# Performance work log

Measured on AMD Instinct MI355X. Metric: run time of the kernel, lower is better.

The kernel has to match this reference:

```python
import jax, jax.numpy as jnp
import numpy as np

MARGIN = 0.7
ITERS = 1000  # as hard-coded in ot_loss's log_optimal_transport call


def setup_inputs() -> dict:
    key = jax.random.key(0)
    k1, k2 = jax.random.split(key)
    # features: N x C x W x H  (query at index 0, 8 targets)
    x = jax.random.normal(k1, (9, 256, 32, 32), dtype=jnp.float32)
    # attention: N x W x H, strictly positive since it is logged directly
    att = jax.random.uniform(k2, (9, 32, 32), dtype=jnp.float32, minval=0.1, maxval=1.0)
    return {"x": x, "att": att, "label": 1}


def _ot_distance(x, att):
    N, C, W, H = x.shape
    m = W * H              # number of query locations
    n = (N - 1) * W * H    # number of target locations
    Q = x[0].reshape(C, m).T                                          # (m, C)
    T = x[1:].reshape(N - 1, C, m).transpose(0, 2, 1).reshape(n, C)   # (n, C)
    mu = att[0].reshape(m)      # query marginal
    nu = att[1:].reshape(n)     # target marginal
    # pairwise squared euclidean distances (m, n)
    M = (jnp.sum(Q * Q, axis=1)[:, None]
         + jnp.sum(T * T, axis=1)[None, :]
         - 2.0 * (Q @ T.T))
    log_mu = jnp.log(mu)
    log_nu = jnp.log(nu)

    def step(carry, _):
        u, v = carry
        u = log_mu - jax.nn.logsumexp(M + v[None, :], axis=1)
        v = log_nu - jax.nn.logsumexp(M + u[:, None], axis=0)
        return (u, v), None

    init = (jnp.zeros((m,), M.dtype), jnp.zeros((n,), M.dtype))
    (u, v), _ = jax.lax.scan(jax.checkpoint(step), init, None, length=ITERS)
    P = jnp.exp(M + u[:, None] + v[None, :])   # transport plan (m, n)
    # OT barycentric distance per query location, summed
    diff = mu[:, None] * Q - P @ T             # (m, C)
    return jnp.sqrt(jnp.sum(diff * diff, axis=1)).sum()


def reference(x, att, label):
    d = _ot_distance(x, att)
    if label:  # label is a concrete python int: positive pair
        return d
    return jnp.clip(MARGIN - d, 0.0, None)
```

## Files before the change

kernel.cpp:

```cpp
#include <hip/hip_runtime.h>
#include <math.h>

#define MR 1024
#define NC 8192
#define NCH 256
#define OT_ITERS 1000
#define IMG_STRIDE 262144

__device__ inline float wredMax(float v){
#pragma unroll
  for (int m = 32; m >= 1; m >>= 1) v = fmaxf(v, __shfl_xor(v, m, 64));
  return v;
}
__device__ inline float wredMin(float v){
#pragma unroll
  for (int m = 32; m >= 1; m >>= 1) v = fminf(v, __shfl_xor(v, m, 64));
  return v;
}
__device__ inline float wredSum(float v){
#pragma unroll
  for (int m = 32; m >= 1; m >>= 1) v += __shfl_xor(v, m, 64);
  return v;
}

__device__ inline unsigned fkey(float f){
  unsigned b = __float_as_uint(f);
  return (b & 0x80000000u) ? ~b : (b | 0x80000000u);
}
__device__ inline float funkey(unsigned k){
  return (k & 0x80000000u) ? __uint_as_float(k & 0x7fffffffu) : __uint_as_float(~k);
}

__global__ __launch_bounds__(256) void kPrep(const float* __restrict__ x,
                                             const float* __restrict__ att,
                                             float* __restrict__ qq, float* __restrict__ tt,
                                             float* __restrict__ logmu, float* __restrict__ lognu,
                                             float* __restrict__ u, float* __restrict__ v,
                                             float* __restrict__ acc, unsigned* __restrict__ prmI){
  int idx = blockIdx.x * 256 + threadIdx.x;
  if (idx < 9216){
    int img = idx >> 10, pos = idx & 1023;
    const float* p = x + img * IMG_STRIDE + pos;
    float s = 0.f;
#pragma unroll 8
    for (int c = 0; c < NCH; ++c){ float a = p[c * 1024]; s += a * a; }
    float lg = logf(att[idx]);
    if (img == 0){ qq[idx] = s;        logmu[idx] = lg; }
    else         { tt[idx - 1024] = s; lognu[idx - 1024] = lg; }
  }
  if (idx < MR) u[idx] = 0.f;
  if (idx < NC) v[idx] = 0.f;
  if (idx == 0){ *acc = 0.f; prmI[0] = 0xFFFFFFFFu; prmI[1] = 0u; }
}

__global__ __launch_bounds__(256) void kGemmM(const float* __restrict__ x,
                                              const float* __restrict__ qq,
                                              const float* __restrict__ tt,
                                              float* __restrict__ M,
                                              unsigned* __restrict__ prmI){
  __shared__ float As[16][68];
  __shared__ float Bs[16][68];
  __shared__ float smn[4], smx[4];
  int jb = blockIdx.x;
  int ib = blockIdx.y;
  int i0 = ib * 64;
  int j0 = jb * 64;
  int k  = j0 >> 10, p0 = j0 & 1023;
  const float* A = x + i0;
  const float* B = x + (1 + k) * IMG_STRIDE + p0;
  int tid = threadIdx.x;
  int lr = tid >> 4, lc = (tid & 15) * 4;
  int ty = tid >> 4, tx = tid & 15;
  float accv[4][4] = {};
  for (int kt = 0; kt < 16; ++kt){
    int c = kt * 16 + lr;
    float4 av = *(const float4*)(A + c * 1024 + lc);
    float4 bv = *(const float4*)(B + c * 1024 + lc);
    *(float4*)(&As[lr][lc]) = av;
    *(float4*)(&Bs[lr][lc]) = bv;
    __syncthreads();
#pragma unroll
    for (int kk = 0; kk < 16; ++kk){
      float4 a = *(const float4*)(&As[kk][ty * 4]);
      float4 b = *(const float4*)(&Bs[kk][tx * 4]);
      float ar[4] = {a.x, a.y, a.z, a.w};
      float br[4] = {b.x, b.y, b.z, b.w};
#pragma unroll
      for (int r = 0; r < 4; ++r)
#pragma unroll
        for (int cc = 0; cc < 4; ++cc) accv[r][cc] += ar[r] * br[cc];
    }
    __syncthreads();
  }
  float tmn = INFINITY, tmx = -INFINITY;
#pragma unroll
  for (int r = 0; r < 4; ++r){
    int i = i0 + ty * 4 + r;
    float qi = qq[i];
    float o[4];
#pragma unroll
    for (int cc = 0; cc < 4; ++cc){
      o[cc] = qi + tt[j0 + tx * 4 + cc] - 2.f * accv[r][cc];
      tmn = fminf(tmn, o[cc]); tmx = fmaxf(tmx, o[cc]);
    }
    float4 ov = { o[0], o[1], o[2], o[3] };
    *(float4*)(M + (long)i * NC + j0 + tx * 4) = ov;
  }
  int lane = tid & 63, w = tid >> 6;
  tmn = wredMin(tmn); tmx = wredMax(tmx);
  if (lane == 0){ smn[w] = tmn; smx[w] = tmx; }
  __syncthreads();
  if (tid == 0){
    float bmn = fminf(fminf(smn[0], smn[1]), fminf(smn[2], smn[3]));
    float bmx = fmaxf(fmaxf(smx[0], smx[1]), fmaxf(smx[2], smx[3]));
    atomicMin(&prmI[0], fkey(bmn));
    atomicMax(&prmI[1], fkey(bmx));
  }
}

__global__ __launch_bounds__(256) void kQuantTrans(const float* __restrict__ M,
                                                   unsigned short* __restrict__ Mq,
                                                   unsigned short* __restrict__ Mtq,
                                                   float* __restrict__ prm){
  __shared__ float tile[64][65];
  const unsigned* prmI = (const unsigned*)prm;
  float mn = funkey(prmI[0]);
  float mx = funkey(prmI[1]);
  float rng = mx - mn;
  float inv = (rng > 0.f) ? 65535.0f / rng : 0.f;
  float sc  = (rng > 0.f) ? rng / 65535.0f : 0.f;
  int i0 = blockIdx.y * 64;
  int j0 = blockIdx.x * 64;
  int t = threadIdx.x;
  int tc = t & 63, tr = t >> 6;
#pragma unroll
  for (int rr = 0; rr < 64; rr += 4)
    tile[rr + tr][tc] = M[(long)(i0 + rr + tr) * NC + j0 + tc];
  __syncthreads();
#pragma unroll
  for (int rr = 0; rr < 64; rr += 4){
    float a = tile[rr + tr][tc];
    int qa = (int)lrintf((a - mn) * inv);
    qa = qa < 0 ? 0 : (qa > 65535 ? 65535 : qa);
    Mq[(long)(i0 + rr + tr) * NC + j0 + tc] = (unsigned short)qa;
    float b = tile[tc][rr + tr];
    int qb = (int)lrintf((b - mn) * inv);
    qb = qb < 0 ? 0 : (qb > 65535 ? 65535 : qb);
    Mtq[(long)(j0 + rr + tr) * MR + i0 + tc] = (unsigned short)qb;
  }
  if (blockIdx.x == 0 && blockIdx.y == 0 && t == 0){ prm[2] = mn; prm[3] = sc; }
}

__global__ __launch_bounds__(256) void kUPassQ(const unsigned short* __restrict__ Mq,
                                               const float* __restrict__ v,
                                               const float* __restrict__ logmu,
                                               float* __restrict__ u,
                                               const float* __restrict__ prm){
  int b = blockIdx.x, tid = threadIdx.x;
  float mn = prm[2], s = prm[3];
  int r0 = 2 * b;
  const unsigned short* R0 = Mq + (long)r0 * NC;
  const unsigned short* R1 = R0 + NC;
  float t0[32], t1[32];
  float mx0 = -INFINITY, mx1 = -INFINITY;
#pragma unroll
  for (int kb = 0; kb < 4; ++kb){
    int cidx = kb * 2048 + tid * 8;
    uint4 qa = *(const uint4*)(R0 + cidx);
    uint4 qb = *(const uint4*)(R1 + cidx);
    float4 v0 = *(const float4*)(v + cidx);
    float4 v1 = *(const float4*)(v + cidx + 4);
    float a0 = fmaf(s, (float)(qa.x & 0xFFFFu), v0.x);
    float a1 = fmaf(s, (float)(qa.x >> 16),     v0.y);
    float a2 = fmaf(s, (float)(qa.y & 0xFFFFu), v0.z);
    float a3 = fmaf(s, (float)(qa.y >> 16),     v0.w);
    float a4 = fmaf(s, (float)(qa.z & 0xFFFFu), v1.x);
    float a5 = fmaf(s, (float)(qa.z >> 16),     v1.y);
    float a6 = fmaf(s, (float)(qa.w & 0xFFFFu), v1.z);
    float a7 = fmaf(s, (float)(qa.w >> 16),     v1.w);
    float c0 = fmaf(s, (float)(qb.x & 0xFFFFu), v0.x);
    float c1 = fmaf(s, (float)(qb.x >> 16),     v0.y);
    float c2 = fmaf(s, (float)(qb.y & 0xFFFFu), v0.z);
    float c3 = fmaf(s, (float)(qb.y >> 16),     v0.w);
    float c4 = fmaf(s, (float)(qb.z & 0xFFFFu), v1.x);
    float c5 = fmaf(s, (float)(qb.z >> 16),     v1.y);
    float c6 = fmaf(s, (float)(qb.w & 0xFFFFu), v1.z);
    float c7 = fmaf(s, (float)(qb.w >> 16),     v1.w);
    t0[kb*8+0]=a0; t0[kb*8+1]=a1; t0[kb*8+2]=a2; t0[kb*8+3]=a3;
    t0[kb*8+4]=a4; t0[kb*8+5]=a5; t0[kb*8+6]=a6; t0[kb*8+7]=a7;
    t1[kb*8+0]=c0; t1[kb*8+1]=c1; t1[kb*8+2]=c2; t1[kb*8+3]=c3;
    t1[kb*8+4]=c4; t1[kb*8+5]=c5; t1[kb*8+6]=c6; t1[kb*8+7]=c7;
    mx0 = fmaxf(mx0, fmaxf(fmaxf(fmaxf(a0,a1),fmaxf(a2,a3)), fmaxf(fmaxf(a4,a5),fmaxf(a6,a7))));
    mx1 = fmaxf(mx1, fmaxf(fmaxf(fmaxf(c0,c1),fmaxf(c2,c3)), fmaxf(fmaxf(c4,c5),fmaxf(c6,c7))));
  }
  __shared__ float redA0[4], redA1[4], redB0[4], redB1[4];
  int lane = tid & 63, w = tid >> 6;
  float wm0 = wredMax(mx0), wm1 = wredMax(mx1);
  if (lane == 0){ redA0[w] = wm0; redA1[w] = wm1; }
  __syncthreads();
  float bm0 = fmaxf(fmaxf(redA0[0], redA0[1]), fmaxf(redA0[2], redA0[3]));
  float bm1 = fmaxf(fmaxf(redA1[0], redA1[1]), fmaxf(redA1[2], redA1[3]));
  float s0 = 0.f, s1 = 0.f;
#pragma unroll
  for (int q = 0; q < 32; ++q){ s0 += __expf(t0[q] - bm0); s1 += __expf(t1[q] - bm1); }
  s0 = wredSum(s0); s1 = wredSum(s1);
  if (lane == 0){ redB0[w] = s0; redB1[w] = s1; }
  __syncthreads();
  if (tid == 0){
    u[r0]     = logmu[r0]     - mn - (bm0 + __logf(redB0[0] + redB0[1] + redB0[2] + redB0[3]));
    u[r0 + 1] = logmu[r0 + 1] - mn - (bm1 + __logf(redB1[0] + redB1[1] + redB1[2] + redB1[3]));
  }
}

__global__ __launch_bounds__(256) void kVPassQ(const unsigned short* __restrict__ Mtq,
                                               const float* __restrict__ u,
                                               const float* __restrict__ lognu,
                                               float* __restrict__ v,
                                               const float* __restrict__ prm){
  __shared__ float ulds[1024];
  int tid = threadIdx.x;
  float mn = prm[2], s = prm[3];
  *(float4*)(&ulds[tid * 4]) = *(const float4*)(u + tid * 4);
  __syncthreads();
  int w = tid >> 6, lane = tid & 63;
#pragma unroll
  for (int cc = 0; cc < 4; ++cc){
    int j = blockIdx.x * 16 + w * 4 + cc;
    const unsigned short* R = Mtq + (long)j * MR;
    uint4 qa = *(const uint4*)(R + lane * 8);
    uint4 qb = *(const uint4*)(R + 512 + lane * 8);
    float4 ua0 = *(const float4*)(&ulds[lane * 8]);
    float4 ua1 = *(const float4*)(&ulds[lane * 8 + 4]);
    float4 ub0 = *(const float4*)(&ulds[512 + lane * 8]);
    float4 ub1 = *(const float4*)(&ulds[512 + lane * 8 + 4]);
    float tv[16];
    tv[0]  = fmaf(s, (float)(qa.x & 0xFFFFu), ua0.x);
    tv[1]  = fmaf(s, (float)(qa.x >> 16),     ua0.y);
    tv[2]  = fmaf(s, (float)(qa.y & 0xFFFFu), ua0.z);
    tv[3]  = fmaf(s, (float)(qa.y >> 16),     ua0.w);
    tv[4]  = fmaf(s, (float)(qa.z & 0xFFFFu), ua1.x);
    tv[5]  = fmaf(s, (float)(qa.z >> 16),     ua1.y);
    tv[6]  = fmaf(s, (float)(qa.w & 0xFFFFu), ua1.z);
    tv[7]  = fmaf(s, (float)(qa.w >> 16),     ua1.w);
    tv[8]  = fmaf(s, (float)(qb.x & 0xFFFFu), ub0.x);
    tv[9]  = fmaf(s, (float)(qb.x >> 16),     ub0.y);
    tv[10] = fmaf(s, (float)(qb.y & 0xFFFFu), ub0.z);
    tv[11] = fmaf(s, (float)(qb.y >> 16),     ub0.w);
    tv[12] = fmaf(s, (float)(qb.z & 0xFFFFu), ub1.x);
    tv[13] = fmaf(s, (float)(qb.z >> 16),     ub1.y);
    tv[14] = fmaf(s, (float)(qb.w & 0xFFFFu), ub1.z);
    tv[15] = fmaf(s, (float)(qb.w >> 16),     ub1.w);
    float mx = -INFINITY;
#pragma unroll
    for (int q = 0; q < 16; ++q) mx = fmaxf(mx, tv[q]);
    mx = wredMax(mx);
    float sm = 0.f;
#pragma unroll
    for (int q = 0; q < 16; ++q) sm += __expf(tv[q] - mx);
    sm = wredSum(sm);
    if (lane == 0) v[j] = lognu[j] - mn - (mx + __logf(sm));
  }
}

__global__ __launch_bounds__(256) void kFinal(const float* __restrict__ x,
                                              const float* __restrict__ att,
                                              const float* __restrict__ M,
                                              const float* __restrict__ u,
                                              const float* __restrict__ v,
                                              float* __restrict__ acc){
  __shared__ float pch[4][256];
  __shared__ float redS[4];
  int tid = threadIdx.x;
  int r0 = blockIdx.x * 4;
  float u4[4];
#pragma unroll
  for (int rr = 0; rr < 4; ++rr) u4[rr] = u[r0 + rr];
  float o[4] = {0.f, 0.f, 0.f, 0.f};
  for (int jc = 0; jc < NC; jc += 256){
    float vv = v[jc + tid];
#pragma unroll
    for (int rr = 0; rr < 4; ++rr)
      pch[rr][tid] = __expf(M[(long)(r0 + rr) * NC + jc + tid] + u4[rr] + vv);
    __syncthreads();
    int k = jc >> 10;
    const float* Tp = x + (1 + k) * IMG_STRIDE + tid * 1024 + (jc & 1023);
    for (int jj = 0; jj < 256; jj += 4){
      float4 tv = *(const float4*)(Tp + jj);
      float tq[4] = {tv.x, tv.y, tv.z, tv.w};
#pragma unroll
      for (int q = 0; q < 4; ++q){
        o[0] += pch[0][jj + q] * tq[q];
        o[1] += pch[1][jj + q] * tq[q];
        o[2] += pch[2][jj + q] * tq[q];
        o[3] += pch[3][jj + q] * tq[q];
      }
    }
    __syncthreads();
  }
  int lane = tid & 63, wid = tid >> 6;
  float dtot = 0.f;
#pragma unroll
  for (int rr = 0; rr < 4; ++rr){
    float mu = att[r0 + rr];
    float qv = x[tid * 1024 + (r0 + rr)];
    float diff = mu * qv - o[rr];
    float wsum = wredSum(diff * diff);
    if (lane == 0) redS[wid] = wsum;
    __syncthreads();
    if (tid == 0) dtot += sqrtf(redS[0] + redS[1] + redS[2] + redS[3]);
    __syncthreads();
  }
  if (tid == 0) atomicAdd(acc, dtot);
}

__global__ void kOut(const float* __restrict__ acc, const int* __restrict__ label,
                     float* __restrict__ out){
  if (threadIdx.x == 0 && blockIdx.x == 0){
    float d = *acc;
    out[0] = (*label) ? d : fmaxf(0.7f - d, 0.f);
  }
}

extern "C" void kernel_launch(void* const* d_in, const int* in_sizes, int n_in,
                              void* d_out, int out_size, void* d_ws, size_t ws_size,
                              hipStream_t stream){
  const float* x   = (const float*)d_in[0];
  const float* att = (const float*)d_in[1];
  const int* label = (const int*)d_in[2];
  float* W = (float*)d_ws;
  float* out = (float*)d_out;

  float* M = W;
  unsigned short* Mq  = (unsigned short*)(W + 8388608);
  unsigned short* Mtq = (unsigned short*)(W + 8388608 + 4194304);
  float* S     = W + 16777216;
  float* qq    = S;
  float* tt    = qq + 1024;
  float* logmu = tt + 8192;
  float* lognu = logmu + 1024;
  float* u     = lognu + 8192;
  float* v     = u + 1024;
  float* acc   = v + 8192;
  float* prm   = acc + 1;
  unsigned* prmI = (unsigned*)prm;

  hipLaunchKernelGGL(kPrep, dim3(37), dim3(256), 0, stream, x, att, qq, tt, logmu, lognu, u, v, acc, prmI);
  hipLaunchKernelGGL(kGemmM, dim3(128, 16), dim3(256), 0, stream, x, qq, tt, M, prmI);
  hipLaunchKernelGGL(kQuantTrans, dim3(128, 16), dim3(256), 0, stream, M, Mq, Mtq, prm);
  for (int it = 0; it < OT_ITERS; ++it){
    hipLaunchKernelGGL(kUPassQ, dim3(512), dim3(256), 0, stream, Mq, v, logmu, u, prm);
    hipLaunchKernelGGL(kVPassQ, dim3(512), dim3(256), 0, stream, Mtq, u, lognu, v, prm);
  }
  hipLaunchKernelGGL(kFinal, dim3(256), dim3(256), 0, stream, x, att, M, u, v, acc);
  hipLaunchKernelGGL(kOut, dim3(1), dim3(1), 0, stream, acc, label, out);
}
```

Measured before the change: 12.50 ms.

## Fuse Sinkhorn iterations into one persistent cooperative kernel with grid barriers

Replaces the 2000 separate u-pass/v-pass kernel launches with a single cooperative persistent kernel of 512 blocks. Each block alternates the u and v log-sum-exp passes and synchronises through a hierarchical atomic grid barrier: 8 groups, each with its own counter and release flag. The aim is to remove per-launch overhead and the inter-kernel drain gaps. The costs are that each block reloads all of v into shared memory every iteration, and spinning barriers depend on all blocks being co-resident. The old launch loop is kept as a fallback if the cooperative launch fails.

```diff
diff --git a/kernel.cpp b/kernel.cpp
--- a/kernel.cpp
+++ b/kernel.cpp
@@ -6,6 +6,7 @@
 #define NCH 256
 #define OT_ITERS 1000
 #define IMG_STRIDE 262144
+#define PBLK 512
 
 __device__ inline float wredMax(float v){
 #pragma unroll
@@ -36,7 +37,8 @@
                                              float* __restrict__ qq, float* __restrict__ tt,
                                              float* __restrict__ logmu, float* __restrict__ lognu,
                                              float* __restrict__ u, float* __restrict__ v,
-                                             float* __restrict__ acc, unsigned* __restrict__ prmI){
+                                             float* __restrict__ acc, unsigned* __restrict__ prmI,
+                                             int* __restrict__ bar){
   int idx = blockIdx.x * 256 + threadIdx.x;
   if (idx < 9216){
     int img = idx >> 10, pos = idx & 1023;
@@ -50,6 +52,7 @@
   }
   if (idx < MR) u[idx] = 0.f;
   if (idx < NC) v[idx] = 0.f;
+  if (idx < 1024) bar[idx] = 0;
   if (idx == 0){ *acc = 0.f; prmI[0] = 0xFFFFFFFFu; prmI[1] = 0u; }
 }
 
@@ -149,6 +152,163 @@
     Mtq[(long)(j0 + rr + tr) * MR + i0 + tc] = (unsigned short)qb;
   }
   if (blockIdx.x == 0 && blockIdx.y == 0 && t == 0){ prm[2] = mn; prm[3] = sc; }
+}
+
+__device__ inline void gbar(int* bar, int g, int ep){
+  __syncthreads();
+  if (threadIdx.x == 0){
+    asm volatile("s_waitcnt vmcnt(0)" ::: "memory");
+    int a = __hip_atomic_fetch_add(&bar[g * 32], 1, __ATOMIC_RELAXED, __HIP_MEMORY_SCOPE_AGENT);
+    if (a == 64 * ep - 1){
+      int go = __hip_atomic_fetch_add(&bar[512], 1, __ATOMIC_RELAXED, __HIP_MEMORY_SCOPE_AGENT);
+      if (go == 8 * ep - 1){
+#pragma unroll
+        for (int g2 = 0; g2 < 8; ++g2)
+          __hip_atomic_store(&bar[256 + g2 * 32], ep, __ATOMIC_RELAXED, __HIP_MEMORY_SCOPE_AGENT);
+      }
+    }
+    while (__hip_atomic_load(&bar[256 + g * 32], __ATOMIC_RELAXED, __HIP_MEMORY_SCOPE_AGENT) < ep)
+      __builtin_amdgcn_s_sleep(4);
+  }
+  __syncthreads();
+}
+
+__global__ __launch_bounds__(256, 2) void kSink2(const unsigned short* __restrict__ Mq,
+                                                 const unsigned short* __restrict__ Mtq,
+                                                 const float* __restrict__ logmu,
+                                                 const float* __restrict__ lognu,
+                                                 float* __restrict__ u,
+                                                 float* __restrict__ v,
+                                                 const float* __restrict__ prm,
+                                                 int* __restrict__ bar){
+  __shared__ float sh[8192];
+  __shared__ float redA0[4], redA1[4], redB0[4], redB1[4];
+  int tid = threadIdx.x, b = blockIdx.x;
+  int lane = tid & 63, w = tid >> 6;
+  int g = b & 7;
+  float mn = prm[2], s = prm[3];
+  int r0 = 2 * b;
+  const unsigned short* R0 = Mq + (long)r0 * NC;
+  const unsigned short* R1 = R0 + NC;
+  float lmu0 = logmu[r0], lmu1 = logmu[r0 + 1];
+  float lnu[4];
+#pragma unroll
+  for (int cc = 0; cc < 4; ++cc) lnu[cc] = lognu[16 * b + w * 4 + cc];
+  int ep = 0;
+
+  for (int it = 0; it < OT_ITERS; ++it){
+#pragma unroll
+    for (int h = 0; h < 2; ++h){
+      float tmp[16];
+#pragma unroll
+      for (int q = 0; q < 16; ++q)
+        tmp[q] = __hip_atomic_load(v + (h * 16 + q) * 256 + tid, __ATOMIC_RELAXED, __HIP_MEMORY_SCOPE_AGENT);
+#pragma unroll
+      for (int q = 0; q < 16; ++q)
+        sh[(h * 16 + q) * 256 + tid] = tmp[q];
+    }
+    __syncthreads();
+    float t0[32], t1[32];
+    float mx0 = -INFINITY, mx1 = -INFINITY;
+#pragma unroll
+    for (int kb = 0; kb < 4; ++kb){
+      int cidx = kb * 2048 + tid * 8;
+      uint4 qa = *(const uint4*)(R0 + cidx);
+      uint4 qb = *(const uint4*)(R1 + cidx);
+      float4 v0 = *(const float4*)(&sh[cidx]);
+      float4 v1 = *(const float4*)(&sh[cidx + 4]);
+      float a0 = fmaf(s, (float)(qa.x & 0xFFFFu), v0.x);
+      float a1 = fmaf(s, (float)(qa.x >> 16),     v0.y);
+      float a2 = fmaf(s, (float)(qa.y & 0xFFFFu), v0.z);
+      float a3 = fmaf(s, (float)(qa.y >> 16),     v0.w);
+      float a4 = fmaf(s, (float)(qa.z & 0xFFFFu), v1.x);
+      float a5 = fmaf(s, (float)(qa.z >> 16),     v1.y);
+      float a6 = fmaf(s, (float)(qa.w & 0xFFFFu), v1.z);
+      float a7 = fmaf(s, (float)(qa.w >> 16),     v1.w);
+      float c0 = fmaf(s, (float)(qb.x & 0xFFFFu), v0.x);
+      float c1 = fmaf(s, (float)(qb.x >> 16),     v0.y);
+      float c2 = fmaf(s, (float)(qb.y & 0xFFFFu), v0.z);
+      float c3 = fmaf(s, (float)(qb.y >> 16),     v0.w);
+      float c4 = fmaf(s, (float)(qb.z & 0xFFFFu), v1.x);
+      float c5 = fmaf(s, (float)(qb.z >> 16),     v1.y);
+      float c6 = fmaf(s, (float)(qb.w & 0xFFFFu), v1.z);
+      float c7 = fmaf(s, (float)(qb.w >> 16),     v1.w);
+      t0[kb*8+0]=a0; t0[kb*8+1]=a1; t0[kb*8+2]=a2; t0[kb*8+3]=a3;
+      t0[kb*8+4]=a4; t0[kb*8+5]=a5; t0[kb*8+6]=a6; t0[kb*8+7]=a7;
+      t1[kb*8+0]=c0; t1[kb*8+1]=c1; t1[kb*8+2]=c2; t1[kb*8+3]=c3;
+      t1[kb*8+4]=c4; t1[kb*8+5]=c5; t1[kb*8+6]=c6; t1[kb*8+7]=c7;
+      mx0 = fmaxf(mx0, fmaxf(fmaxf(fmaxf(a0,a1),fmaxf(a2,a3)), fmaxf(fmaxf(a4,a5),fmaxf(a6,a7))));
+      mx1 = fmaxf(mx1, fmaxf(fmaxf(fmaxf(c0,c1),fmaxf(c2,c3)), fmaxf(fmaxf(c4,c5),fmaxf(c6,c7))));
+    }
+    float wm0 = wredMax(mx0), wm1 = wredMax(mx1);
+    if (lane == 0){ redA0[w] = wm0; redA1[w] = wm1; }
+    __syncthreads();
+    float bm0 = fmaxf(fmaxf(redA0[0], redA0[1]), fmaxf(redA0[2], redA0[3]));
+    float bm1 = fmaxf(fmaxf(redA1[0], redA1[1]), fmaxf(redA1[2], redA1[3]));
+    float s0 = 0.f, s1 = 0.f;
+#pragma unroll
+    for (int q = 0; q < 32; ++q){ s0 += __expf(t0[q] - bm0); s1 += __expf(t1[q] - bm1); }
+    s0 = wredSum(s0); s1 = wredSum(s1);
+    if (lane == 0){ redB0[w] = s0; redB1[w] = s1; }
+    __syncthreads();
+    if (tid == 0){
+      float nu0 = lmu0 - mn - (bm0 + __logf(redB0[0] + redB0[1] + redB0[2] + redB0[3]));
+      float nu1 = lmu1 - mn - (bm1 + __logf(redB1[0] + redB1[1] + redB1[2] + redB1[3]));
+      __hip_atomic_store(u + r0,     nu0, __ATOMIC_RELAXED, __HIP_MEMORY_SCOPE_AGENT);
+      __hip_atomic_store(u + r0 + 1, nu1, __ATOMIC_RELAXED, __HIP_MEMORY_SCOPE_AGENT);
+    }
+    gbar(bar, g, ++ep);
+
+    {
+      float tu[4];
+#pragma unroll
+      for (int q = 0; q < 4; ++q)
+        tu[q] = __hip_atomic_load(u + q * 256 + tid, __ATOMIC_RELAXED, __HIP_MEMORY_SCOPE_AGENT);
+#pragma unroll
+      for (int q = 0; q < 4; ++q) sh[q * 256 + tid] = tu[q];
+    }
+    __syncthreads();
+#pragma unroll
+    for (int cc = 0; cc < 4; ++cc){
+      int j = 16 * b + w * 4 + cc;
+      const unsigned short* R = Mtq + (long)j * MR;
+      uint4 qa = *(const uint4*)(R + lane * 8);
+      uint4 qb = *(const uint4*)(R + 512 + lane * 8);
+      float4 ua0 = *(const float4*)(&sh[lane * 8]);
+      float4 ua1 = *(const float4*)(&sh[lane * 8 + 4]);
+      float4 ub0 = *(const float4*)(&sh[512 + lane * 8]);
+      float4 ub1 = *(const float4*)(&sh[512 + lane * 8 + 4]);
+      float tv[16];
+      tv[0]  = fmaf(s, (float)(qa.x & 0xFFFFu), ua0.x);
+      tv[1]  = fmaf(s, (float)(qa.x >> 16),     ua0.y);
+      tv[2]  = fmaf(s, (float)(qa.y & 0xFFFFu), ua0.z);
+      tv[3]  = fmaf(s, (float)(qa.y >> 16),     ua0.w);
+      tv[4]  = fmaf(s, (float)(qa.z & 0xFFFFu), ua1.x);
+      tv[5]  = fmaf(s, (float)(qa.z >> 16),     ua1.y);
+      tv[6]  = fmaf(s, (float)(qa.w & 0xFFFFu), ua1.z);
+      tv[7]  = fmaf(s, (float)(qa.w >> 16),     ua1.w);
+      tv[8]  = fmaf(s, (float)(qb.x & 0xFFFFu), ub0.x);
+      tv[9]  = fmaf(s, (float)(qb.x >> 16),     ub0.y);
+      tv[10] = fmaf(s, (float)(qb.y & 0xFFFFu), ub0.z);
+      tv[11] = fmaf(s, (float)(qb.y >> 16),     ub0.w);
+      tv[12] = fmaf(s, (float)(qb.z & 0xFFFFu), ub1.x);
+      tv[13] = fmaf(s, (float)(qb.z >> 16),     ub1.y);
+      tv[14] = fmaf(s, (float)(qb.w & 0xFFFFu), ub1.z);
+      tv[15] = fmaf(s, (float)(qb.w >> 16),     ub1.w);
+      float mx = -INFINITY;
+#pragma unroll
+      for (int q = 0; q < 16; ++q) mx = fmaxf(mx, tv[q]);
+      mx = wredMax(mx);
+      float sm = 0.f;
+#pragma unroll
+      for (int q = 0; q < 16; ++q) sm += __expf(tv[q] - mx);
+      sm = wredSum(sm);
+      if (lane == 0)
+        __hip_atomic_store(v + j, lnu[cc] - mn - (mx + __logf(sm)),
+                           __ATOMIC_RELAXED, __HIP_MEMORY_SCOPE_AGENT);
+    }
+    gbar(bar, g, ++ep);
+  }
 }
 
 __global__ __launch_bounds__(256) void kUPassQ(const unsigned short* __restrict__ Mq,
@@ -343,13 +503,21 @@
   float* acc   = v + 8192;
   float* prm   = acc + 1;
   unsigned* prmI = (unsigned*)prm;
-
-  hipLaunchKernelGGL(kPrep, dim3(37), dim3(256), 0, stream, x, att, qq, tt, logmu, lognu, u, v, acc, prmI);
+  int*   bar   = (int*)(prm + 4);
+
+  hipLaunchKernelGGL(kPrep, dim3(37), dim3(256), 0, stream, x, att, qq, tt, logmu, lognu, u, v, acc, prmI, bar);
   hipLaunchKernelGGL(kGemmM, dim3(128, 16), dim3(256), 0, stream, x, qq, tt, M, prmI);
   hipLaunchKernelGGL(kQuantTrans, dim3(128, 16), dim3(256), 0, stream, M, Mq, Mtq, prm);
-  for (int it = 0; it < OT_ITERS; ++it){
-    hipLaunchKernelGGL(kUPassQ, dim3(512), dim3(256), 0, stream, Mq, v, logmu, u, prm);
-    hipLaunchKernelGGL(kVPassQ, dim3(512), dim3(256), 0, stream, Mtq, u, lognu, v, prm);
+
+  void* args[] = { (void*)&Mq, (void*)&Mtq, (void*)&logmu, (void*)&lognu,
+                   (void*)&u, (void*)&v, (void*)&prm, (void*)&bar };
+  hipError_t rc = hipLaunchCooperativeKernel((const void*)kSink2,
+                                             dim3(PBLK), dim3(256), args, 0, stream);
+  if (rc != hipSuccess){
+    for (int it = 0; it < OT_ITERS; ++it){
+      hipLaunchKernelGGL(kUPassQ, dim3(512), dim3(256), 0, stream, Mq, v, logmu, u, prm);
+      hipLaunchKernelGGL(kVPassQ, dim3(512), dim3(256), 0, stream, Mtq, u, lognu, v, prm);
+    }
   }
   hipLaunchKernelGGL(kFinal, dim3(256), dim3(256), 0, stream, x, att, M, u, v, acc);
   hipLaunchKernelGGL(kOut, dim3(1), dim3(1), 0, stream, acc, label, out);
```

New measurement: 11.88 ms. -5.0%, faster.

## Fuse Sinkhorn iterations into one persistent cooperative kernel with grid barriers

Applied to the files above, without the earlier changes.

Replaces the 2000 separate u/v pass kernel launches with a single cooperative persistent kernel of 256 blocks. The blocks synchronise through a hierarchical atomic grid barrier and read each other's updates with cache-bypassing loads. The kernel also reuses the previous iteration's log-sum as a stabiliser, so the max pass is skipped unless the sum overflows or underflows, and it works in base-2 exponentials. This removes launch overhead and per-iteration max reductions, at the cost of spin-barrier latency, correctness that depends on cross-block memory visibility, and co-residency of all blocks.

```diff
diff --git a/kernel.cpp b/kernel.cpp
--- a/kernel.cpp
+++ b/kernel.cpp
@@ -6,6 +6,9 @@
 #define NCH 256
 #define OT_ITERS 1000
 #define IMG_STRIDE 262144
+#define PBLK 256
+#define L2EF 1.44269504088896340736f
+#define LN2F 0.69314718055994530942f
 
 __device__ inline float wredMax(float v){
 #pragma unroll
@@ -29,6 +32,28 @@
 }
 __device__ inline float funkey(unsigned k){
   return (k & 0x80000000u) ? __uint_as_float(k & 0x7fffffffu) : __uint_as_float(~k);
+}
+
+__device__ inline float4 cload_f4(const float4* p){
+  float4 r;
+  asm volatile("global_load_dwordx4 %0, %1, off sc0 sc1\n\ts_waitcnt vmcnt(0)"
+               : "=v"(r) : "v"(p) : "memory");
+  return r;
+}
+__device__ inline void cload_f4x4(float4* r, const float4* p0, const float4* p1,
+                                  const float4* p2, const float4* p3){
+  asm volatile(
+    "global_load_dwordx4 %0, %4, off sc0 sc1\n\t"
+    "global_load_dwordx4 %1, %5, off sc0 sc1\n\t"
+    "global_load_dwordx4 %2, %6, off sc0 sc1\n\t"
+    "global_load_dwordx4 %3, %7, off sc0 sc1\n\t"
+    "s_waitcnt vmcnt(0)"
+    : "=&v"(r[0]), "=&v"(r[1]), "=&v"(r[2]), "=v"(r[3])
+    : "v"(p0), "v"(p1), "v"(p2), "v"(p3)
+    : "memory");
+}
+__device__ inline void astore(float* p, float val){
+  __hip_atomic_store(p, val, __ATOMIC_RELAXED, __HIP_MEMORY_SCOPE_AGENT);
 }
 
 __global__ __launch_bounds__(256) void kPrep(const float* __restrict__ x,
@@ -36,7 +61,8 @@
                                              float* __restrict__ qq, float* __restrict__ tt,
                                              float* __restrict__ logmu, float* __restrict__ lognu,
                                              float* __restrict__ u, float* __restrict__ v,
-                                             float* __restrict__ acc, unsigned* __restrict__ prmI){
+                                             float* __restrict__ acc, unsigned* __restrict__ prmI,
+                                             int* __restrict__ bar){
   int idx = blockIdx.x * 256 + threadIdx.x;
   if (idx < 9216){
     int img = idx >> 10, pos = idx & 1023;
@@ -50,6 +76,7 @@
   }
   if (idx < MR) u[idx] = 0.f;
   if (idx < NC) v[idx] = 0.f;
+  if (idx < 1024) bar[idx] = 0;
   if (idx == 0){ *acc = 0.f; prmI[0] = 0xFFFFFFFFu; prmI[1] = 0u; }
 }
 
@@ -149,6 +176,187 @@
     Mtq[(long)(j0 + rr + tr) * MR + i0 + tc] = (unsigned short)qb;
   }
   if (blockIdx.x == 0 && blockIdx.y == 0 && t == 0){ prm[2] = mn; prm[3] = sc; }
+}
+
+__device__ inline void gbar(int* bar, int g, int ep){
+  __syncthreads();
+  if (threadIdx.x == 0){
+    asm volatile("s_waitcnt vmcnt(0)" ::: "memory");
+    int a = __hip_atomic_fetch_add(&bar[g * 32], 1, __ATOMIC_RELAXED, __HIP_MEMORY_SCOPE_AGENT);
+    if (a == 32 * ep - 1){
+      int go = __hip_atomic_fetch_add(&bar[512], 1, __ATOMIC_RELAXED, __HIP_MEMORY_SCOPE_AGENT);
+      if (go == 8 * ep - 1){
+#pragma unroll
+        for (int g2 = 0; g2 < 8; ++g2)
+          __hip_atomic_store(&bar[256 + g2 * 32], ep, __ATOMIC_RELAXED, __HIP_MEMORY_SCOPE_AGENT);
+      }
+    }
+    while (__hip_atomic_load(&bar[256 + g * 32], __ATOMIC_RELAXED, __HIP_MEMORY_SCOPE_AGENT) < ep)
+      __builtin_amdgcn_s_sleep(1);
+  }
+  __syncthreads();
+}
+
+__device__ inline float bredSum8(float* red, float x, int lane, int w){
+  x = wredSum(x);
+  __syncthreads();
+  if (lane == 0) red[w] = x;
+  __syncthreads();
+  return ((red[0] + red[1]) + (red[2] + red[3])) + ((red[4] + red[5]) + (red[6] + red[7]));
+}
+__device__ inline float bredMax8(float* red, float x, int lane, int w){
+  x = wredMax(x);
+  __syncthreads();
+  if (lane == 0) red[w] = x;
+  __syncthreads();
+  return fmaxf(fmaxf(fmaxf(red[0], red[1]), fmaxf(red[2], red[3])),
+               fmaxf(fmaxf(red[4], red[5]), fmaxf(red[6], red[7])));
+}
+
+__global__ __launch_bounds__(512) void kSink3(const unsigned short* __restrict__ Mq,
+                                              const unsigned short* __restrict__ Mtq,
+                                              const float* __restrict__ logmu,
+                                              const float* __restrict__ lognu,
+                                              float* __restrict__ u,
+                                              float* __restrict__ v,
+                                              const float* __restrict__ prm,
+                                              int* __restrict__ bar){
+  __shared__ float shu[1024];
+  __shared__ float red[8];
+  int tid = threadIdx.x, b = blockIdx.x;
+  int lane = tid & 63, w = tid >> 6;
+  int g = b & 7;
+  float mn = prm[2], s = prm[3];
+  float s2 = s * L2EF;
+  int r0 = 4 * b;
+  float lmu[4];
+#pragma unroll
+  for (int r = 0; r < 4; ++r) lmu[r] = logmu[r0 + r];
+  int jb = 32 * b + 4 * w;
+  float lnu[4];
+#pragma unroll
+  for (int c = 0; c < 4; ++c) lnu[c] = lognu[jb + c];
+  float B2u[4] = {0.f, 0.f, 0.f, 0.f};
+  float B2v[4] = {0.f, 0.f, 0.f, 0.f};
+  int ep = 0;
+
+  for (int it = 0; it < OT_ITERS; ++it){
+    const float4* vp = (const float4*)v;
+    float4 vb[4];
+    cload_f4x4(vb, vp + 2 * tid, vp + 2 * tid + 1, vp + 1024 + 2 * tid, vp + 1024 + 2 * tid + 1);
+#pragma unroll
+    for (int k = 0; k < 4; ++k){
+      vb[k].x *= L2EF; vb[k].y *= L2EF; vb[k].z *= L2EF; vb[k].w *= L2EF;
+    }
+#pragma unroll
+    for (int r = 0; r < 4; ++r){
+      const unsigned short* Rr = Mq + (long)(r0 + r) * NC;
+      float Lv = 0.f;
+      bool redo = true;
+      if (it >= 2){
+        float b2 = B2u[r];
+        float part = 0.f;
+#pragma unroll
+        for (int h = 0; h < 2; ++h){
+          uint4 q = *(const uint4*)(Rr + 4096 * h + 8 * tid);
+          float4 v0 = vb[2 * h], v1 = vb[2 * h + 1];
+          part += __builtin_exp2f(fmaf(s2, (float)(q.x & 0xFFFFu), v0.x) - b2);
+          part += __builtin_exp2f(fmaf(s2, (float)(q.x >> 16),     v0.y) - b2);
+          part += __builtin_exp2f(fmaf(s2, (float)(q.y & 0xFFFFu), v0.z) - b2);
+          part += __builtin_exp2f(fmaf(s2, (float)(q.y >> 16),     v0.w) - b2);
+          part += __builtin_exp2f(fmaf(s2, (float)(q.z & 0xFFFFu), v1.x) - b2);
+          part += __builtin_exp2f(fmaf(s2, (float)(q.z >> 16),     v1.y) - b2);
+          part += __builtin_exp2f(fmaf(s2, (float)(q.w & 0xFFFFu), v1.z) - b2);
+          part += __builtin_exp2f(fmaf(s2, (float)(q.w >> 16),     v1.w) - b2);
+        }
+        float tot = bredSum8(red, part, lane, w);
+        redo = !(tot > 0.f && tot < 3.0e38f);
+        Lv = b2 + __builtin_log2f(tot);
+      }
+      if (redo){
+        float tv[16];
+        float mx = -INFINITY;
+#pragma unroll
+        for (int h = 0; h < 2; ++h){
+          uint4 q = *(const uint4*)(Rr + 4096 * h + 8 * tid);
+          float4 v0 = vb[2 * h], v1 = vb[2 * h + 1];
+          tv[h*8+0] = fmaf(s2, (float)(q.x & 0xFFFFu), v0.x);
+          tv[h*8+1] = fmaf(s2, (float)(q.x >> 16),     v0.y);
+          tv[h*8+2] = fmaf(s2, (float)(q.y & 0xFFFFu), v0.z);
+          tv[h*8+3] = fmaf(s2, (float)(q.y >> 16),     v0.w);
+          tv[h*8+4] = fmaf(s2, (float)(q.z & 0xFFFFu), v1.x);
+          tv[h*8+5] = fmaf(s2, (float)(q.z >> 16),     v1.y);
+          tv[h*8+6] = fmaf(s2, (float)(q.w & 0xFFFFu), v1.z);
+          tv[h*8+7] = fmaf(s2, (float)(q.w >> 16),     v1.w);
+#pragma unroll
+          for (int e = 0; e < 8; ++e) mx = fmaxf(mx, tv[h*8+e]);
+        }
+        float bmx = bredMax8(red, mx, lane, w);
+        float p2 = 0.f;
+#pragma unroll
+        for (int q2 = 0; q2 < 16; ++q2) p2 += __builtin_exp2f(tv[q2] - bmx);
+        float tot2 = bredSum8(red, p2, lane, w);
+        Lv = bmx + __builtin_log2f(tot2);
+      }
+      B2u[r] = Lv;
+      if (tid == 0) astore(u + r0 + r, lmu[r] - mn - Lv * LN2F);
+    }
+    gbar(bar, g, ++ep);
+
+    if (tid < 256){
+      float4 uu = cload_f4((const float4*)u + tid);
+      uu.x *= L2EF; uu.y *= L2EF; uu.z *= L2EF; uu.w *= L2EF;
+      *(float4*)(&shu[tid * 4]) = uu;
+    }
+    __syncthreads();
+    float4 uf[4];
+#pragma unroll
+    for (int k = 0; k < 4; ++k) uf[k] = *(const float4*)(&shu[4 * (k * 64 + lane)]);
+#pragma unroll
+    for (int c = 0; c < 4; ++c){
+      int j = jb + c;
+      const unsigned short* Rc = Mtq + (long)j * MR;
+      float Lv = 0.f;
+      bool redo = true;
+      if (it >= 2){
+        float b2 = B2v[c];
+        float part = 0.f;
+#pragma unroll
+        for (int k = 0; k < 4; ++k){
+          uint2 q = *(const uint2*)(Rc + 4 * (k * 64 + lane));
+          part += __builtin_exp2f(fmaf(s2, (float)(q.x & 0xFFFFu), uf[k].x) - b2);
+          part += __builtin_exp2f(fmaf(s2, (float)(q.x >> 16),     uf[k].y) - b2);
+          part += __builtin_exp2f(fmaf(s2, (float)(q.y & 0xFFFFu), uf[k].z) - b2);
+          part += __builtin_exp2f(fmaf(s2, (float)(q.y >> 16),     uf[k].w) - b2);
+        }
+        float tot = wredSum(part);
+        redo = !(tot > 0.f && tot < 3.0e38f);
+        Lv = b2 + __builtin_log2f(tot);
+      }
+      if (redo){
+        float tvv[16];
+        float mx = -INFINITY;
+#pragma unroll
+        for (int k = 0; k < 4; ++k){
+          uint2 q = *(const uint2*)(Rc + 4 * (k * 64 + lane));
+          tvv[k*4+0] = fmaf(s2, (float)(q.x & 0xFFFFu), uf[k].x);
+          tvv[k*4+1] = fmaf(s2, (float)(q.x >> 16),     uf[k].y);
+          tvv[k*4+2] = fmaf(s2, (float)(q.y & 0xFFFFu), uf[k].z);
+          tvv[k*4+3] = fmaf(s2, (float)(q.y >> 16),     uf[k].w);
+          mx = fmaxf(mx, fmaxf(fmaxf(tvv[k*4], tvv[k*4+1]), fmaxf(tvv[k*4+2], tvv[k*4+3])));
+        }
+        mx = wredMax(mx);
+        float p2 = 0.f;
+#pragma unroll
+        for (int q2 = 0; q2 < 16; ++q2) p2 += __builtin_exp2f(tvv[q2] - mx);
+        p2 = wredSum(p2);
+        Lv = mx + __builtin_log2f(p2);
+      }
+      B2v[c] = Lv;
+      if (lane == 0) astore(v + j, lnu[c] - mn - Lv * LN2F);
+    }
+    gbar(bar, g, ++ep);
+  }
 }
 
 __global__ __launch_bounds__(256) void kUPassQ(const unsigned short* __restrict__ Mq,
@@ -343,13 +551,21 @@
   float* acc   = v + 8192;
   float* prm   = acc + 1;
   unsigned* prmI = (unsigned*)prm;
-
-  hipLaunchKernelGGL(kPrep, dim3(37), dim3(256), 0, stream, x, att, qq, tt, logmu, lognu, u, v, acc, prmI);
+  int*   bar   = (int*)(prm + 4);
+
+  hipLaunchKernelGGL(kPrep, dim3(37), dim3(256), 0, stream, x, att, qq, tt, logmu, lognu, u, v, acc, prmI, bar);
   hipLaunchKernelGGL(kGemmM, dim3(128, 16), dim3(256), 0, stream, x, qq, tt, M, prmI);
   hipLaunchKernelGGL(kQuantTrans, dim3(128, 16), dim3(256), 0, stream, M, Mq, Mtq, prm);
-  for (int it = 0; it < OT_ITERS; ++it){
-    hipLaunchKernelGGL(kUPassQ, dim3(512), dim3(256), 0, stream, Mq, v, logmu, u, prm);
-    hipLaunchKernelGGL(kVPassQ, dim3(512), dim3(256), 0, stream, Mtq, u, lognu, v, prm);
+
+  void* args[] = { (void*)&Mq, (void*)&Mtq, (void*)&logmu, (void*)&lognu,
+                   (void*)&u, (void*)&v, (void*)&prm, (void*)&bar };
+  hipError_t rc = hipLaunchCooperativeKernel((const void*)kSink3,
+                                             dim3(PBLK), dim3(512), args, 0, stream);
+  if (rc != hipSuccess){
+    for (int it = 0; it < OT_ITERS; ++it){
+      hipLaunchKernelGGL(kUPassQ, dim3(512), dim3(256), 0, stream, Mq, v, logmu, u, prm);
+      hipLaunchKernelGGL(kVPassQ, dim3(512), dim3(256), 0, stream, Mtq, u, lognu, v, prm);
+    }
   }
   hipLaunchKernelGGL(kFinal, dim3(256), dim3(256), 0, stream, x, att, M, u, v, acc);
   hipLaunchKernelGGL(kOut, dim3(1), dim3(1), 0, stream, acc, label, out);
```

Result: slower. 15.15 ms (+21.2%).

## Fuse Sinkhorn iterations into persistent cooperative kernel with sparse candidate lists

Applied to the files above, without the earlier changes.

Replaces the 2000 per-iteration kernel launches with one persistent cooperative kernel that uses a hierarchical global barrier between the u and v half-steps. After a warmup, each row and column periodically rebuilds a shared-memory list of entries within a fixed margin of the running max and runs logsumexp only over those entries, falling back to the dense pass when a list overflows. This is meant to remove launch overhead and most of the exp and memory traffic per iteration. In exchange it approximates logsumexp by dropping terms below the margin, and stale candidate lists between rebuilds could introduce error.

```diff
diff --git a/kernel.cpp b/kernel.cpp
--- a/kernel.cpp
+++ b/kernel.cpp
@@ -6,6 +6,13 @@
 #define NCH 256
 #define OT_ITERS 1000
 #define IMG_STRIDE 262144
+#define PBLK 256
+#define L2EF 1.44269504088896340736f
+#define LN2F 0.69314718055994530942f
+#define CAPR 768
+#define CAPC 384
+#define MARG2 40.0f
+#define WARMUP 16
 
 __device__ inline float wredMax(float v){
 #pragma unroll
@@ -29,6 +36,13 @@
 }
 __device__ inline float funkey(unsigned k){
   return (k & 0x80000000u) ? __uint_as_float(k & 0x7fffffffu) : __uint_as_float(~k);
+}
+
+__device__ inline float aload(const float* p){
+  return __hip_atomic_load(p, __ATOMIC_RELAXED, __HIP_MEMORY_SCOPE_AGENT);
+}
+__device__ inline void astore(float* p, float val){
+  __hip_atomic_store(p, val, __ATOMIC_RELAXED, __HIP_MEMORY_SCOPE_AGENT);
 }
 
 __global__ __launch_bounds__(256) void kPrep(const float* __restrict__ x,
@@ -36,7 +50,8 @@
                                              float* __restrict__ qq, float* __restrict__ tt,
                                              float* __restrict__ logmu, float* __restrict__ lognu,
                                              float* __restrict__ u, float* __restrict__ v,
-                                             float* __restrict__ acc, unsigned* __restrict__ prmI){
+                                             float* __restrict__ acc, unsigned* __restrict__ prmI,
+                                             int* __restrict__ bar){
   int idx = blockIdx.x * 256 + threadIdx.x;
   if (idx < 9216){
     int img = idx >> 10, pos = idx & 1023;
@@ -50,6 +65,7 @@
   }
   if (idx < MR) u[idx] = 0.f;
   if (idx < NC) v[idx] = 0.f;
+  if (idx < 1024) bar[idx] = 0;
   if (idx == 0){ *acc = 0.f; prmI[0] = 0xFFFFFFFFu; prmI[1] = 0u; }
 }
 
@@ -149,6 +165,216 @@
     Mtq[(long)(j0 + rr + tr) * MR + i0 + tc] = (unsigned short)qb;
   }
   if (blockIdx.x == 0 && blockIdx.y == 0 && t == 0){ prm[2] = mn; prm[3] = sc; }
+}
+
+__device__ inline void gbar(int* bar, int g, int ep){
+  __syncthreads();
+  if (threadIdx.x == 0){
+    asm volatile("s_waitcnt vmcnt(0)" ::: "memory");
+    int a = __hip_atomic_fetch_add(&bar[g * 32], 1, __ATOMIC_RELAXED, __HIP_MEMORY_SCOPE_AGENT);
+    if (a == 32 * ep - 1){
+      int go = __hip_atomic_fetch_add(&bar[512], 1, __ATOMIC_RELAXED, __HIP_MEMORY_SCOPE_AGENT);
+      if (go == 8 * ep - 1){
+#pragma unroll
+        for (int g2 = 0; g2 < 8; ++g2)
+          __hip_atomic_store(&bar[256 + g2 * 32], ep, __ATOMIC_RELAXED, __HIP_MEMORY_SCOPE_AGENT);
+      }
+    }
+    while (__hip_atomic_load(&bar[256 + g * 32], __ATOMIC_RELAXED, __HIP_MEMORY_SCOPE_AGENT) < ep)
+      __builtin_amdgcn_s_sleep(1);
+  }
+  __syncthreads();
+}
+
+__global__ __launch_bounds__(512) void kSink4(const float* __restrict__ M,
+                                              const unsigned short* __restrict__ Mtq,
+                                              const float* __restrict__ logmu,
+                                              const float* __restrict__ lognu,
+                                              float* __restrict__ u,
+                                              float* __restrict__ v,
+                                              const float* __restrict__ prm,
+                                              int* __restrict__ bar){
+  __shared__ unsigned rowl[4 * CAPR];
+  __shared__ unsigned coll[32 * CAPC];
+  __shared__ float red[16];
+  __shared__ int cnts[36];
+  int tid = threadIdx.x, b = blockIdx.x;
+  int lane = tid & 63, w = tid >> 6;
+  int g = b & 7;
+  float mn = prm[2], s = prm[3];
+  float s2 = s * L2EF;
+  float inv = (s > 0.f) ? 1.0f / s : 0.f;
+  int r0 = 4 * b;
+  int jb0 = 32 * b;
+  int r = w >> 1;
+  int idx = (w & 1) * 64 + lane;
+  int i_row = r0 + r;
+  const float* Mr = M + (long)i_row * NC;
+  float lmu_r = logmu[i_row];
+  float lnu4[4];
+#pragma unroll
+  for (int cc = 0; cc < 4; ++cc) lnu4[cc] = lognu[jb0 + w * 4 + cc];
+
+  if (tid < 36) cnts[tid] = -1;
+  __syncthreads();
+  int ep = 0;
+
+  for (int it = 0; it < OT_ITERS; ++it){
+    bool rebuild = (it >= WARMUP) && (((it - WARMUP) & 63) == 0);
+
+    if (rebuild){
+      if (tid < 36) cnts[tid] = 0;
+      __syncthreads();
+      float mxb = -INFINITY;
+      for (int k = 0; k < 64; ++k){
+        int j = idx + k * 128;
+        float a = (Mr[j] - mn) + aload(v + j);
+        mxb = fmaxf(mxb, a);
+      }
+      mxb = wredMax(mxb);
+      if (lane == 0) red[w] = mxb;
+      __syncthreads();
+      float thr = fmaxf(red[2 * r], red[2 * r + 1]) - MARG2 * LN2F;
+      for (int k = 0; k < 64; ++k){
+        int j = idx + k * 128;
+        float mv = Mr[j] - mn;
+        float a = mv + aload(v + j);
+        if (a >= thr){
+          int p = atomicAdd(&cnts[r], 1);
+          if (p < CAPR){
+            int qv = (int)lrintf(mv * inv);
+            qv = qv < 0 ? 0 : (qv > 65535 ? 65535 : qv);
+            rowl[r * CAPR + p] = ((unsigned)qv << 13) | (unsigned)j;
+          }
+        }
+      }
+      __syncthreads();
+      if (tid < 4 && cnts[tid] > CAPR) cnts[tid] = -1;
+      __syncthreads();
+    }
+
+    {
+      int cnt = cnts[r];
+      float t2v[6];
+      float mx = -INFINITY;
+      if (cnt >= 0){
+#pragma unroll
+        for (int q = 0; q < 6; ++q){
+          int e = idx + q * 128;
+          bool act = (e < cnt);
+          unsigned ent = rowl[r * CAPR + (act ? e : 0)];
+          int j = act ? (int)(ent & 8191u) : 0;
+          float vj = aload(v + j);
+          float t2 = act ? fmaf(s2, (float)(ent >> 13), L2EF * vj) : -INFINITY;
+          t2v[q] = t2;
+          mx = fmaxf(mx, t2);
+        }
+      } else {
+        for (int k = 0; k < 64; ++k){
+          int j = idx + k * 128;
+          float a = (Mr[j] - mn) + aload(v + j);
+          mx = fmaxf(mx, a * L2EF);
+        }
+      }
+      mx = wredMax(mx);
+      if (lane == 0) red[w] = mx;
+      __syncthreads();
+      float bmx = fmaxf(red[2 * r], red[2 * r + 1]);
+      float sm = 0.f;
+      if (cnt >= 0){
+#pragma unroll
+        for (int q = 0; q < 6; ++q) sm += __builtin_exp2f(t2v[q] - bmx);
+      } else {
+        for (int k = 0; k < 64; ++k){
+          int j = idx + k * 128;
+          float a = (Mr[j] - mn) + aload(v + j);
+          sm += __builtin_exp2f(a * L2EF - bmx);
+        }
+      }
+      sm = wredSum(sm);
+      if (lane == 0) red[8 + w] = sm;
+      __syncthreads();
+      if (idx == 0){
+        float tot = red[8 + 2 * r] + red[8 + 2 * r + 1];
+        float Lv = bmx + __builtin_log2f(tot);
+        astore(u + i_row, lmu_r - mn - Lv * LN2F);
+      }
+    }
+    gbar(bar, g, ++ep);
+
+    if (rebuild){
+#pragma unroll
+      for (int cc = 0; cc < 4; ++cc){
+        int cj = w * 4 + cc;
+        const unsigned short* Rc = Mtq + (long)(jb0 + cj) * MR;
+        float mx = -INFINITY;
+        for (int k = 0; k < 16; ++k){
+          int i = lane + k * 64;
+          float t2 = fmaf(s2, (float)Rc[i], L2EF * aload(u + i));
+          mx = fmaxf(mx, t2);
+        }
+        mx = wredMax(mx);
+        float thr = mx - MARG2;
+        for (int k = 0; k < 16; ++k){
+          int i = lane + k * 64;
+          float qv = (float)Rc[i];
+          float t2 = fmaf(s2, qv, L2EF * aload(u + i));
+          if (t2 >= thr){
+            int p = atomicAdd(&cnts[4 + cj], 1);
+            if (p < CAPC) coll[cj * CAPC + p] = ((unsigned)Rc[i] << 10) | (unsigned)i;
+          }
+        }
+      }
+      __syncthreads();
+      if (tid >= 4 && tid < 36 && cnts[tid] > CAPC) cnts[tid] = -1;
+      __syncthreads();
+    }
+
+#pragma unroll
+    for (int cc = 0; cc < 4; ++cc){
+      int cj = w * 4 + cc;
+      int j = jb0 + cj;
+      int cnt = cnts[4 + cj];
+      float t2v[6];
+      float mx = -INFINITY;
+      if (cnt >= 0){
+#pragma unroll
+        for (int q = 0; q < 6; ++q){
+          int e = lane + q * 64;
+          bool act = (e < cnt);
+          unsigned ent = coll[cj * CAPC + (act ? e : 0)];
+          int i = act ? (int)(ent & 1023u) : 0;
+          float ui = aload(u + i);
+          float t2 = act ? fmaf(s2, (float)(ent >> 10), L2EF * ui) : -INFINITY;
+          t2v[q] = t2;
+          mx = fmaxf(mx, t2);
+        }
+        mx = wredMax(mx);
+        float sm = 0.f;
+#pragma unroll
+        for (int q = 0; q < 6; ++q) sm += __builtin_exp2f(t2v[q] - mx);
+        sm = wredSum(sm);
+        if (lane == 0) astore(v + j, lnu4[cc] - mn - (mx + __builtin_log2f(sm)) * LN2F);
+      } else {
+        const unsigned short* Rc = Mtq + (long)j * MR;
+        for (int k = 0; k < 16; ++k){
+          int i = lane + k * 64;
+          float t2 = fmaf(s2, (float)Rc[i], L2EF * aload(u + i));
+          mx = fmaxf(mx, t2);
+        }
+        mx = wredMax(mx);
+        float sm = 0.f;
+        for (int k = 0; k < 16; ++k){
+          int i = lane + k * 64;
+          float t2 = fmaf(s2, (float)Rc[i], L2EF * aload(u + i));
+          sm += __builtin_exp2f(t2 - mx);
+        }
+        sm = wredSum(sm);
+        if (lane == 0) astore(v + j, lnu4[cc] - mn - (mx + __builtin_log2f(sm)) * LN2F);
+      }
+    }
+    gbar(bar, g, ++ep);
+  }
 }
 
 __global__ __launch_bounds__(256) void kUPassQ(const unsigned short* __restrict__ Mq,
@@ -343,13 +569,21 @@
   float* acc   = v + 8192;
   float* prm   = acc + 1;
   unsigned* prmI = (unsigned*)prm;
-
-  hipLaunchKernelGGL(kPrep, dim3(37), dim3(256), 0, stream, x, att, qq, tt, logmu, lognu, u, v, acc, prmI);
+  int*   bar   = (int*)(prm + 4);
+
+  hipLaunchKernelGGL(kPrep, dim3(37), dim3(256), 0, stream, x, att, qq, tt, logmu, lognu, u, v, acc, prmI, bar);
   hipLaunchKernelGGL(kGemmM, dim3(128, 16), dim3(256), 0, stream, x, qq, tt, M, prmI);
   hipLaunchKernelGGL(kQuantTrans, dim3(128, 16), dim3(256), 0, stream, M, Mq, Mtq, prm);
-  for (int it = 0; it < OT_ITERS; ++it){
-    hipLaunchKernelGGL(kUPassQ, dim3(512), dim3(256), 0, stream, Mq, v, logmu, u, prm);
-    hipLaunchKernelGGL(kVPassQ, dim3(512), dim3(256), 0, stream, Mtq, u, lognu, v, prm);
+
+  void* args[] = { (void*)&M, (void*)&Mtq, (void*)&logmu, (void*)&lognu,
+                   (void*)&u, (void*)&v, (void*)&prm, (void*)&bar };
+  hipError_t rc = hipLaunchCooperativeKernel((const void*)kSink4,
+                                             dim3(PBLK), dim3(512), args, 0, stream);
+  if (rc != hipSuccess){
+    for (int it = 0; it < OT_ITERS; ++it){
+      hipLaunchKernelGGL(kUPassQ, dim3(512), dim3(256), 0, stream, Mq, v, logmu, u, prm);
+      hipLaunchKernelGGL(kVPassQ, dim3(512), dim3(256), 0, stream, Mtq, u, lognu, v, prm);
+    }
   }
   hipLaunchKernelGGL(kFinal, dim3(256), dim3(256), 0, stream, x, att, M, u, v, acc);
   hipLaunchKernelGGL(kOut, dim3(1), dim3(1), 0, stream, acc, label, out);
```

New measurement: 12.91 ms. 3.3% more time.
